# Optimization experiments

Measured on AMD Instinct MI355X. Metric: run time of the kernel, lower is better.

The kernel has to match this reference:

```python
import jax, jax.numpy as jnp
import numpy as np

B, S, D, H = 2, 2048, 1024, 16
DEPTH = D // H


def setup_inputs() -> dict:
    key = jax.random.key(0)
    ks = jax.random.split(key, 12)
    sc = 1.0 / np.sqrt(D)
    n = lambda k, shp, s=sc: jax.random.normal(k, shp, dtype=jnp.float32) * s
    return {
        "q": jax.random.normal(ks[0], (B, S, D), dtype=jnp.float32),
        "k": jax.random.normal(ks[1], (B, S, D), dtype=jnp.float32),
        "v": jax.random.normal(ks[2], (B, S, D), dtype=jnp.float32),
        # key-padding mask: 1 = masked, 0 = keep (added to logits * -1e9)
        "mask": (jax.random.uniform(ks[3], (B, 1, 1, S)) < 0.1).astype(jnp.float32),
        "wq_w": n(ks[4], (D, D)), "wq_b": jnp.zeros((D,), jnp.float32),
        "wk_w": n(ks[5], (D, D)), "wk_b": jnp.zeros((D,), jnp.float32),
        "wv_w": n(ks[6], (D, D)), "wv_b": jnp.zeros((D,), jnp.float32),
        "dense_w": n(ks[7], (D, D)), "dense_b": jnp.zeros((D,), jnp.float32),
    }


def _split_heads(x, b, s):
    # [B, S, D] -> [B, H, S, depth]
    return x.reshape(b, s, H, DEPTH).transpose(0, 2, 1, 3)


def reference(q, k, v, mask, wq_w, wq_b, wk_w, wk_b, wv_w, wv_b, dense_w, dense_b):
    b, sq, _ = q.shape
    sk = k.shape[1]
    qh = _split_heads(q @ wq_w.T + wq_b, b, sq)
    kh = _split_heads(k @ wk_w.T + wk_b, b, sk)
    vh = _split_heads(v @ wv_w.T + wv_b, b, sk)
    scale = 1.0 / jnp.sqrt(jnp.float32(DEPTH))
    logits = jnp.einsum('bhqd,bhkd->bhqk', qh, kh) * scale  # [B,H,Sq,Sk]
    logits = logits + mask * (-1e9)
    attn = jax.nn.softmax(logits, axis=-1)
    ctx = jnp.einsum('bhqk,bhkd->bhqd', attn, vh)
    ctx = ctx.transpose(0, 2, 1, 3).reshape(b, sq, D)  # concat heads
    out = ctx @ dense_w.T + dense_b
    return out, attn
```

## Files before the change

### kernel.cpp

```cpp
#include <hip/hip_runtime.h>

#define BB 2
#define SS 2048
#define DD 1024
#define HH 16
#define DEPTH 64
#define MTOT (BB*SS)
#define QW 8
#define QBLK (QW*16)
#define NT (SS/64)
#define NT2 (SS/128)
#define NPROJ ((size_t)BB*HH*SS*DEPTH)
#define WSZ   ((size_t)DD*DD)

using f16 = _Float16;
typedef _Float16 f16x8 __attribute__((ext_vector_type(8)));
typedef _Float16 f16x4 __attribute__((ext_vector_type(4)));
typedef float f32x4 __attribute__((ext_vector_type(4)));

#define LOG2E 1.44269504088896f
#define SC2   (0.125f * LOG2E)

#define GLOAD16(g, l) __builtin_amdgcn_global_load_lds(                      \
    (__attribute__((address_space(1))) const void*)(g),                      \
    (__attribute__((address_space(3))) void*)(l), 16, 0, 0)

__global__ __launch_bounds__(256) void cvt_kernel(
    const float* __restrict__ q, const float* __restrict__ k, const float* __restrict__ v,
    const float* __restrict__ w0, const float* __restrict__ w1, const float* __restrict__ w2,
    f16* __restrict__ qf, f16* __restrict__ kf, f16* __restrict__ vf,
    f16* __restrict__ wq, f16* __restrict__ wk, f16* __restrict__ wv)
{
    const int z = blockIdx.y;
    const float* s = z==0?q : z==1?k : z==2?v : z==3?w0 : z==4?w1 : w2;
    f16*        d = z==0?qf: z==1?kf: z==2?vf: z==3?wq: z==4?wk: wv;
    const size_t n = (z < 3) ? NPROJ : WSZ;
    for (size_t i = ((size_t)blockIdx.x * 256 + threadIdx.x) * 8; i < n;
         i += (size_t)gridDim.x * 256 * 8) {
        f32x4 a = *(const f32x4*)(s + i);
        f32x4 b = *(const f32x4*)(s + i + 4);
        f16x8 o = {(f16)a[0], (f16)a[1], (f16)a[2], (f16)a[3],
                   (f16)b[0], (f16)b[1], (f16)b[2], (f16)b[3]};
        *(f16x8*)(d + i) = o;
    }
}

__global__ __launch_bounds__(256) void cvt2_kernel(
    const float* __restrict__ s, f16* __restrict__ d)
{
    size_t i = ((size_t)blockIdx.x * 256 + threadIdx.x) * 8;
    if (i < WSZ) {
        f32x4 a = *(const f32x4*)(s + i);
        f32x4 b = *(const f32x4*)(s + i + 4);
        f16x8 o = {(f16)a[0], (f16)a[1], (f16)a[2], (f16)a[3],
                   (f16)b[0], (f16)b[1], (f16)b[2], (f16)b[3]};
        *(f16x8*)(d + i) = o;
    }
}

__global__ __launch_bounds__(256, 4) void proj_kernel(
    const f16* __restrict__ qf, const f16* __restrict__ kf, const f16* __restrict__ vf,
    const f16* __restrict__ wqw, const f16* __restrict__ wkw, const f16* __restrict__ wvw,
    const float* __restrict__ bq, const float* __restrict__ bk, const float* __restrict__ bv,
    f16* __restrict__ qh, f16* __restrict__ kh, f16* __restrict__ vt)
{
    const int mode = blockIdx.z;
    const f16* A    = mode==0 ? qf  : mode==1 ? kf  : vf;
    const f16* Bw   = mode==0 ? wqw : mode==1 ? wkw : wvw;
    const float* bias = mode==0 ? bq : mode==1 ? bk : bv;

    __shared__ f16 As[128*64];
    __shared__ f16 Bs[128*64];

    const int tid = threadIdx.x, wave = tid >> 6, lane = tid & 63;
    const int m0 = blockIdx.y * 128, n0 = blockIdx.x * 128;
    const int wm = (wave >> 1) * 64, wn = (wave & 1) * 64;
    const int lrow = lane & 15, g = lane >> 4;
    const int sw = lrow & 7;
    const int srow = tid >> 3;
    const int schk = (tid & 7) ^ (srow & 7);

    f32x4 acc[4][4] = {};

    for (int kk = 0; kk < DD; kk += 64) {
        #pragma unroll
        for (int i = 0; i < 4; ++i) {
            GLOAD16(A  + (size_t)(m0 + i*32 + srow) * DD + kk + schk * 8,
                    &As[i*2048 + wave*512]);
            GLOAD16(Bw + (size_t)(n0 + i*32 + srow) * DD + kk + schk * 8,
                    &Bs[i*2048 + wave*512]);
        }
        __syncthreads();
        for (int kf2 = 0; kf2 < 2; ++kf2) {
            f16x8 a[4], bf[4];
            for (int i = 0; i < 4; ++i)
                a[i]  = *(const f16x8*)&As[(wm + i*16 + lrow)*64 + ((kf2*4 + g) ^ sw)*8];
            for (int i = 0; i < 4; ++i)
                bf[i] = *(const f16x8*)&Bs[(wn + i*16 + lrow)*64 + ((kf2*4 + g) ^ sw)*8];
            for (int mi = 0; mi < 4; ++mi)
                for (int ni = 0; ni < 4; ++ni)
                    acc[mi][ni] = __builtin_amdgcn_mfma_f32_16x16x32_f16(a[mi], bf[ni], acc[mi][ni], 0, 0, 0);
        }
        __syncthreads();
    }

    const int rbase = g * 4;
    if (mode == 2) {
        for (int ni = 0; ni < 4; ++ni) {
            int n = n0 + wn + ni * 16 + lrow;
            float bval = bias[n];
            int hh = n >> 6, dep = n & 63;
            for (int mi = 0; mi < 4; ++mi) {
                int m = m0 + wm + mi * 16 + rbase;
                int bb = m >> 11, s = m & 2047;
                f16x4 pk = {(f16)(acc[mi][ni][0] + bval), (f16)(acc[mi][ni][1] + bval),
                            (f16)(acc[mi][ni][2] + bval), (f16)(acc[mi][ni][3] + bval)};
                *(f16x4*)&vt[((size_t)(bb * HH + hh) * DEPTH + dep) * SS + s] = pk;
            }
        }
    } else {
        f16* dst = (mode == 0) ? qh : kh;
        for (int ni = 0; ni < 4; ++ni) {
            int n = n0 + wn + ni * 16 + lrow;
            float bval = bias[n];
            int hh = n >> 6, dep = n & 63;
            for (int mi = 0; mi < 4; ++mi)
                for (int j = 0; j < 4; ++j) {
                    int m = m0 + wm + mi * 16 + rbase + j;
                    int bb = m >> 11, s = m & 2047;
                    dst[((size_t)(bb * HH + hh) * SS + s) * DEPTH + dep] = (f16)(acc[mi][ni][j] + bval);
                }
        }
    }
}

__global__ __launch_bounds__(512, 6) void attn_kernel(
    const f16* __restrict__ qh, const f16* __restrict__ kh, const f16* __restrict__ vt,
    const float* __restrict__ mask, float* __restrict__ attn_out, f16* __restrict__ ctx)
{
    __shared__ unsigned char mflag[SS];
    __shared__ f16 Ks[2][64*64];
    __shared__ f16 Vs[2][64*64];
    __shared__ f16 Pl[QW][16][72];

    const int tid = threadIdx.x, wave = tid >> 6, lane = tid & 63;
    const int L = blockIdx.x;
    const int xcd = L & 7, iw = L >> 3;
    const int bh = xcd * 4 + (iw >> 4);
    const int qb = iw & 15;
    const int b = bh >> 4, h = bh & 15;
    const int q0 = qb * QBLK;
    const int lrow = lane & 15, g = lane >> 4;
    const int rbase = g * 4;
    const int sw = lrow & 7;
    const int srow = tid >> 3;
    const int schk = (tid & 7) ^ (srow & 7);

    const f16* Qbase = qh + (size_t)bh * SS * DEPTH;
    const f16* Kb = kh + (size_t)bh * SS * DEPTH;
    const f16* Vb = vt + (size_t)bh * DEPTH * SS;

    for (int i = tid; i < SS; i += 512)
        mflag[i] = mask[b * SS + i] > 0.5f ? 1 : 0;

    f16x8 aq[2];
    for (int kf2 = 0; kf2 < 2; ++kf2)
        aq[kf2] = *(const f16x8*)(Qbase + (size_t)(q0 + wave*16 + lrow) * DEPTH + kf2*32 + g*8);

    float s_l[4] = {0.f, 0.f, 0.f, 0.f};
    GLOAD16(Kb + (size_t)(srow) * DEPTH + schk * 8,        &Ks[0][wave * 512]);
    GLOAD16(Kb + (size_t)(64 + srow) * DEPTH + schk * 8,   &Vs[0][wave * 512]);
    __syncthreads();
    for (int t = 0; t < NT2; ++t) {
        const int cur = t & 1;
        if (t + 1 < NT2) {
            GLOAD16(Kb + (size_t)((t+1)*128 + srow) * DEPTH + schk * 8,      &Ks[cur ^ 1][wave * 512]);
            GLOAD16(Kb + (size_t)((t+1)*128 + 64 + srow) * DEPTH + schk * 8, &Vs[cur ^ 1][wave * 512]);
        }
        #pragma unroll
        for (int nf = 0; nf < 8; ++nf) {
            const f16* tb = (nf < 4) ? &Ks[cur][0] : &Vs[cur][0];
            const int nfl = nf & 3;
            f32x4 a4 = {};
            for (int kf2 = 0; kf2 < 2; ++kf2) {
                f16x8 bf = *(const f16x8*)&tb[(nfl*16 + lrow)*64 + ((kf2*4 + g) ^ sw)*8];
                a4 = __builtin_amdgcn_mfma_f32_16x16x32_f16(aq[kf2], bf, a4, 0, 0, 0);
            }
            float sel = mflag[t*128 + nf*16 + lrow] ? 0.f : 1.f;
            for (int j = 0; j < 4; ++j)
                s_l[j] += sel * __builtin_amdgcn_exp2f(a4[j] * SC2);
        }
        __syncthreads();
    }
    for (int j = 0; j < 4; ++j) {
        float s = s_l[j];
        for (int off = 1; off < 16; off <<= 1) s += __shfl_xor(s, off);
        s_l[j] = 1.0f / s;
    }

    f32x4 cacc[4] = {};
    f32x4 st[4];
    float* arow = attn_out + ((size_t)bh * SS + q0 + wave * 16) * SS;
    GLOAD16(Kb + (size_t)(0*64 + srow) * DEPTH + schk * 8, &Ks[0][wave * 512]);
    GLOAD16(Vb + (size_t)srow * SS + 0*64 + schk * 8,      &Vs[0][wave * 512]);
    __syncthreads();
    for (int kt = 0; kt < NT; ++kt) {
        const int cur = kt & 1;
        if (kt > 0) {
            #pragma unroll
            for (int i = 0; i < 4; ++i) {
                int r = i * 4 + g;
                __builtin_nontemporal_store(st[i],
                    (f32x4*)&arow[(size_t)r * SS + (kt-1)*64 + lrow*4]);
            }
        }
        if (kt + 1 < NT) {
            GLOAD16(Kb + (size_t)((kt+1)*64 + srow) * DEPTH + schk * 8, &Ks[cur ^ 1][wave * 512]);
            GLOAD16(Vb + (size_t)srow * SS + (kt+1)*64 + schk * 8,      &Vs[cur ^ 1][wave * 512]);
        }
        for (int nf = 0; nf < 4; ++nf) {
            f32x4 a4 = {};
            for (int kf2 = 0; kf2 < 2; ++kf2) {
                f16x8 bf = *(const f16x8*)&Ks[cur][(nf*16 + lrow)*64 + ((kf2*4 + g) ^ sw)*8];
                a4 = __builtin_amdgcn_mfma_f32_16x16x32_f16(aq[kf2], bf, a4, 0, 0, 0);
            }
            float sel = mflag[kt*64 + nf*16 + lrow] ? 0.f : 1.f;
            for (int j = 0; j < 4; ++j) {
                float p = sel * __builtin_amdgcn_exp2f(a4[j] * SC2) * s_l[j];
                Pl[wave][rbase + j][nf*16 + lrow] = (f16)p;
            }
        }
        for (int kf2 = 0; kf2 < 2; ++kf2) {
            f16x8 pa = *(const f16x8*)&Pl[wave][lrow][kf2*32 + g*8];
            for (int nf = 0; nf < 4; ++nf) {
                f16x8 bv = *(const f16x8*)&Vs[cur][(nf*16 + lrow)*64 + ((kf2*4 + g) ^ sw)*8];
                cacc[nf] = __builtin_amdgcn_mfma_f32_16x16x32_f16(pa, bv, cacc[nf], 0, 0, 0);
            }
        }
        #pragma unroll
        for (int i = 0; i < 4; ++i) {
            int r = i * 4 + g;
            f16x4 pv4 = *(const f16x4*)&Pl[wave][r][lrow * 4];
            st[i] = (f32x4){(float)pv4[0], (float)pv4[1], (float)pv4[2], (float)pv4[3]};
        }
        __syncthreads();
    }
    #pragma unroll
    for (int i = 0; i < 4; ++i) {
        int r = i * 4 + g;
        __builtin_nontemporal_store(st[i],
            (f32x4*)&arow[(size_t)r * SS + (NT-1)*64 + lrow*4]);
    }
    for (int nf = 0; nf < 4; ++nf)
        for (int j = 0; j < 4; ++j) {
            int qrow = q0 + wave * 16 + rbase + j;
            ctx[((size_t)(b * SS + qrow) * HH + h) * DEPTH + nf*16 + lrow] = (f16)cacc[nf][j];
        }
}

__global__ __launch_bounds__(256, 4) void dense_kernel(
    const f16* __restrict__ ctx, const f16* __restrict__ W16,
    const float* __restrict__ bias, float* __restrict__ out)
{
    __shared__ f16 As[128*64];
    __shared__ f16 Bs[128*64];

    const int tid = threadIdx.x, wave = tid >> 6, lane = tid & 63;
    const int m0 = blockIdx.y * 128, n0 = blockIdx.x * 128;
    const int wm = (wave >> 1) * 64, wn = (wave & 1) * 64;
    const int lrow = lane & 15, g = lane >> 4;
    const int sw = lrow & 7;
    const int srow = tid >> 3;
    const int schk = (tid & 7) ^ (srow & 7);

    f32x4 acc[4][4] = {};

    for (int kk = 0; kk < DD; kk += 64) {
        #pragma unroll
        for (int i = 0; i < 4; ++i) {
            GLOAD16(ctx + (size_t)(m0 + i*32 + srow) * DD + kk + schk * 8,
                    &As[i*2048 + wave*512]);
            GLOAD16(W16 + (size_t)(n0 + i*32 + srow) * DD + kk + schk * 8,
                    &Bs[i*2048 + wave*512]);
        }
        __syncthreads();
        for (int kf2 = 0; kf2 < 2; ++kf2) {
            f16x8 a[4], bf[4];
            for (int i = 0; i < 4; ++i)
                a[i]  = *(const f16x8*)&As[(wm + i*16 + lrow)*64 + ((kf2*4 + g) ^ sw)*8];
            for (int i = 0; i < 4; ++i)
                bf[i] = *(const f16x8*)&Bs[(wn + i*16 + lrow)*64 + ((kf2*4 + g) ^ sw)*8];
            for (int mi = 0; mi < 4; ++mi)
                for (int ni = 0; ni < 4; ++ni)
                    acc[mi][ni] = __builtin_amdgcn_mfma_f32_16x16x32_f16(a[mi], bf[ni], acc[mi][ni], 0, 0, 0);
        }
        __syncthreads();
    }

    const int rbase = g * 4;
    for (int ni = 0; ni < 4; ++ni) {
        int n = n0 + wn + ni * 16 + lrow;
        float bval = bias[n];
        for (int mi = 0; mi < 4; ++mi)
            for (int j = 0; j < 4; ++j) {
                int m = m0 + wm + mi * 16 + rbase + j;
                out[(size_t)m * DD + n] = acc[mi][ni][j] + bval;
            }
    }
}

extern "C" void kernel_launch(void* const* d_in, const int* in_sizes, int n_in,
                              void* d_out, int out_size, void* d_ws, size_t ws_size,
                              hipStream_t stream) {
    const float* q       = (const float*)d_in[0];
    const float* k       = (const float*)d_in[1];
    const float* v       = (const float*)d_in[2];
    const float* mask    = (const float*)d_in[3];
    const float* wq_w    = (const float*)d_in[4];
    const float* wq_b    = (const float*)d_in[5];
    const float* wk_w    = (const float*)d_in[6];
    const float* wk_b    = (const float*)d_in[7];
    const float* wv_w    = (const float*)d_in[8];
    const float* wv_b    = (const float*)d_in[9];
    const float* dense_w = (const float*)d_in[10];
    const float* dense_b = (const float*)d_in[11];

    float* out  = (float*)d_out;
    float* attn = out + (size_t)MTOT * DD;

    f16* qh  = (f16*)d_ws;
    f16* kh  = qh + NPROJ;
    f16* vt  = kh + NPROJ;
    f16* ctx = vt + NPROJ;

    f16* sc   = (f16*)attn;
    f16* qf   = sc;
    f16* kf   = sc + NPROJ;
    f16* vf   = sc + 2*NPROJ;
    f16* wq16 = sc + 3*NPROJ;
    f16* wk16 = wq16 + WSZ;
    f16* wv16 = wk16 + WSZ;

    f16* dw16 = qh;

    cvt_kernel<<<dim3(1024, 6), 256, 0, stream>>>(q, k, v, wq_w, wk_w, wv_w,
                                                  qf, kf, vf, wq16, wk16, wv16);
    proj_kernel<<<dim3(8, 32, 3), 256, 0, stream>>>(qf, kf, vf, wq16, wk16, wv16,
                                                    wq_b, wk_b, wv_b, qh, kh, vt);
    attn_kernel<<<dim3(512), 512, 0, stream>>>(qh, kh, vt, mask, attn, ctx);
    cvt2_kernel<<<dim3(512), 256, 0, stream>>>(dense_w, dw16);
    dense_kernel<<<dim3(8, 32), 256, 0, stream>>>(ctx, dw16, dense_b, out);
}
```

Measured before the change: 222.3 us.

## Triple-buffer K/V tiles in attention with partial vmcnt barrier waits

Grows the shared K/V staging in both attention passes from double to triple buffering. Each tile is now prefetched two iterations ahead. The full __syncthreads at the end of each iteration becomes a custom barrier that waits only until the older async global-to-LDS loads have landed (vmcnt 2 or 6), so newer loads and attention stores stay in flight. This aims to hide global-load latency better. In exchange it uses more LDS, lowers the launch-bounds occupancy hint from 6 to 4, and issues redundant wrap-around loads on the final iterations.

```diff
diff --git a/kernel.cpp b/kernel.cpp
--- a/kernel.cpp
+++ b/kernel.cpp
@@ -25,6 +25,14 @@
     (__attribute__((address_space(1))) const void*)(g),                      \
     (__attribute__((address_space(3))) void*)(l), 16, 0, 0)
 
+#define BARV(N) do {                                                         \
+    __builtin_amdgcn_sched_barrier(0);                                       \
+    asm volatile("s_waitcnt vmcnt(" #N ") lgkmcnt(0)" ::: "memory");         \
+    __builtin_amdgcn_sched_barrier(0);                                       \
+    __builtin_amdgcn_s_barrier();                                            \
+    __builtin_amdgcn_sched_barrier(0);                                       \
+} while (0)
+
 __global__ __launch_bounds__(256) void cvt_kernel(
     const float* __restrict__ q, const float* __restrict__ k, const float* __restrict__ v,
     const float* __restrict__ w0, const float* __restrict__ w1, const float* __restrict__ w2,
@@ -134,13 +142,13 @@
     }
 }
 
-__global__ __launch_bounds__(512, 6) void attn_kernel(
+__global__ __launch_bounds__(512, 4) void attn_kernel(
     const f16* __restrict__ qh, const f16* __restrict__ kh, const f16* __restrict__ vt,
     const float* __restrict__ mask, float* __restrict__ attn_out, f16* __restrict__ ctx)
 {
     __shared__ unsigned char mflag[SS];
-    __shared__ f16 Ks[2][64*64];
-    __shared__ f16 Vs[2][64*64];
+    __shared__ f16 Ks[3][64*64];
+    __shared__ f16 Vs[3][64*64];
     __shared__ f16 Pl[QW][16][72];
 
     const int tid = threadIdx.x, wave = tid >> 6, lane = tid & 63;
@@ -170,13 +178,15 @@
     float s_l[4] = {0.f, 0.f, 0.f, 0.f};
     GLOAD16(Kb + (size_t)(srow) * DEPTH + schk * 8,        &Ks[0][wave * 512]);
     GLOAD16(Kb + (size_t)(64 + srow) * DEPTH + schk * 8,   &Vs[0][wave * 512]);
+    GLOAD16(Kb + (size_t)(128 + srow) * DEPTH + schk * 8,  &Ks[1][wave * 512]);
+    GLOAD16(Kb + (size_t)(192 + srow) * DEPTH + schk * 8,  &Vs[1][wave * 512]);
     __syncthreads();
     for (int t = 0; t < NT2; ++t) {
-        const int cur = t & 1;
-        if (t + 1 < NT2) {
-            GLOAD16(Kb + (size_t)((t+1)*128 + srow) * DEPTH + schk * 8,      &Ks[cur ^ 1][wave * 512]);
-            GLOAD16(Kb + (size_t)((t+1)*128 + 64 + srow) * DEPTH + schk * 8, &Vs[cur ^ 1][wave * 512]);
-        }
+        const int cur = t % 3;
+        const int nxt = (t + 2) % 3;
+        const int t2 = (t + 2) & (NT2 - 1);
+        GLOAD16(Kb + (size_t)(t2*128 + srow) * DEPTH + schk * 8,      &Ks[nxt][wave * 512]);
+        GLOAD16(Kb + (size_t)(t2*128 + 64 + srow) * DEPTH + schk * 8, &Vs[nxt][wave * 512]);
         #pragma unroll
         for (int nf = 0; nf < 8; ++nf) {
             const f16* tb = (nf < 4) ? &Ks[cur][0] : &Vs[cur][0];
@@ -190,7 +200,8 @@
             for (int j = 0; j < 4; ++j)
                 s_l[j] += sel * __builtin_amdgcn_exp2f(a4[j] * SC2);
         }
-        __syncthreads();
+        if (t < NT2 - 1) BARV(2);
+        else __syncthreads();
     }
     for (int j = 0; j < 4; ++j) {
         float s = s_l[j];
@@ -201,11 +212,15 @@
     f32x4 cacc[4] = {};
     f32x4 st[4];
     float* arow = attn_out + ((size_t)bh * SS + q0 + wave * 16) * SS;
-    GLOAD16(Kb + (size_t)(0*64 + srow) * DEPTH + schk * 8, &Ks[0][wave * 512]);
-    GLOAD16(Vb + (size_t)srow * SS + 0*64 + schk * 8,      &Vs[0][wave * 512]);
+    GLOAD16(Kb + (size_t)(srow) * DEPTH + schk * 8,        &Ks[0][wave * 512]);
+    GLOAD16(Vb + (size_t)srow * SS + 0 + schk * 8,         &Vs[0][wave * 512]);
+    GLOAD16(Kb + (size_t)(64 + srow) * DEPTH + schk * 8,   &Ks[1][wave * 512]);
+    GLOAD16(Vb + (size_t)srow * SS + 64 + schk * 8,        &Vs[1][wave * 512]);
     __syncthreads();
     for (int kt = 0; kt < NT; ++kt) {
-        const int cur = kt & 1;
+        const int cur = kt % 3;
+        const int nxt = (kt + 2) % 3;
+        const int t2 = (kt + 2) & (NT - 1);
         if (kt > 0) {
             #pragma unroll
             for (int i = 0; i < 4; ++i) {
@@ -214,10 +229,8 @@
                     (f32x4*)&arow[(size_t)r * SS + (kt-1)*64 + lrow*4]);
             }
         }
-        if (kt + 1 < NT) {
-            GLOAD16(Kb + (size_t)((kt+1)*64 + srow) * DEPTH + schk * 8, &Ks[cur ^ 1][wave * 512]);
-            GLOAD16(Vb + (size_t)srow * SS + (kt+1)*64 + schk * 8,      &Vs[cur ^ 1][wave * 512]);
-        }
+        GLOAD16(Kb + (size_t)(t2*64 + srow) * DEPTH + schk * 8, &Ks[nxt][wave * 512]);
+        GLOAD16(Vb + (size_t)srow * SS + t2*64 + schk * 8,      &Vs[nxt][wave * 512]);
         for (int nf = 0; nf < 4; ++nf) {
             f32x4 a4 = {};
             for (int kf2 = 0; kf2 < 2; ++kf2) {
@@ -243,7 +256,7 @@
             f16x4 pv4 = *(const f16x4*)&Pl[wave][r][lrow * 4];
             st[i] = (f32x4){(float)pv4[0], (float)pv4[1], (float)pv4[2], (float)pv4[3]};
         }
-        __syncthreads();
+        BARV(6);
     }
     #pragma unroll
     for (int i = 0; i < 4; ++i) {
```

New measurement: 218.9 us. Within noise of the previous version (-1.5%).
